# Optimization experiments

Hardware: AMD Instinct MI355X
Metric: run time of the kernel (lower is better)

Reference implementation:

```python
import jax, jax.numpy as jnp
import numpy as np

H = 2048        # hidden_size
NH = 16         # num query heads
NKV = 4         # num kv heads
HD = 128        # head_dim
EPS = 1e-6
SCALE = HD ** -0.5
GROUPS = NH // NKV


def rotate_half(x):
    x1, x2 = x[..., : HD // 2], x[..., HD // 2:]
    return jnp.concatenate((-x2, x1), axis=-1)


def rmsnorm(x, w):
    # x: [..., HD]
    var = jnp.mean(jnp.square(x), axis=-1, keepdims=True)
    return x * jax.lax.rsqrt(var + EPS) * w


def setup_inputs() -> dict:
    key = jax.random.key(0)
    ks = jax.random.split(key, 10)
    B, QL, CL = 4, 1024, 3072
    s = 0.02
    return {
        "noise": jax.random.normal(ks[0], (B, QL, H), jnp.float32),
        "ctx": jax.random.normal(ks[1], (B, CL, H), jnp.float32),
        "cos": jax.random.uniform(ks[2], (B, CL + QL, HD), jnp.float32, -1.0, 1.0),
        "sin": jax.random.uniform(ks[3], (B, CL + QL, HD), jnp.float32, -1.0, 1.0),
        "Wq": jax.random.normal(ks[4], (H, NH * HD), jnp.float32) * s,
        "Wk": jax.random.normal(ks[5], (H, NKV * HD), jnp.float32) * s,
        "Wv": jax.random.normal(ks[6], (H, NKV * HD), jnp.float32) * s,
        "Wo": jax.random.normal(ks[7], (NH * HD, H), jnp.float32) * s,
        "qn_w": jnp.ones((HD,), jnp.float32),
        "kn_w": jnp.ones((HD,), jnp.float32),
    }


def reference(noise, ctx, cos, sin, Wq, Wk, Wv, Wo, qn_w, kn_w):
    B, QL, _ = noise.shape
    CL = ctx.shape[1]
    KL = CL + QL

    # Q from noise
    q = (noise @ Wq).reshape(B, QL, NH, HD)
    q = rmsnorm(q, qn_w).transpose(0, 2, 1, 3)            # [B, NH, QL, HD]

    # K/V from [ctx ; noise]
    kv_in = jnp.concatenate([ctx, noise], axis=1)          # [B, KL, H]
    k = (kv_in @ Wk).reshape(B, KL, NKV, HD)
    k = rmsnorm(k, kn_w).transpose(0, 2, 1, 3)             # [B, NKV, KL, HD]
    v = (kv_in @ Wv).reshape(B, KL, NKV, HD).transpose(0, 2, 1, 3)

    # RoPE: queries use last QL positions
    cos_q, sin_q = cos[:, -QL:, None].transpose(0, 2, 1, 3), sin[:, -QL:, None].transpose(0, 2, 1, 3)
    cos_k, sin_k = cos[:, None], sin[:, None]
    q = q * cos_q + rotate_half(q) * sin_q
    k = k * cos_k + rotate_half(k) * sin_k

    # GQA expansion
    k = jnp.repeat(k, GROUPS, axis=1)                      # [B, NH, KL, HD]
    v = jnp.repeat(v, GROUPS, axis=1)

    attn = jnp.einsum('bhqd,bhkd->bhqk', q, k) * SCALE     # [B, NH, QL, KL]
    attn = jax.nn.softmax(attn.astype(jnp.float32), axis=-1).astype(v.dtype)
    out = jnp.einsum('bhqk,bhkd->bhqd', attn, v)
    out = out.transpose(0, 2, 1, 3).reshape(B, QL, NH * HD)
    return out @ Wo
```

## Files before the change

### kernel.cpp

```cpp
#include <hip/hip_runtime.h>
#include <cstdint>
#include <cstddef>

#define DEVI __device__ __forceinline__

typedef short bf16x8 __attribute__((ext_vector_type(8)));
typedef short bf16x4 __attribute__((ext_vector_type(4)));
typedef float f32x4  __attribute__((ext_vector_type(4)));

constexpr int H_  = 2048;
constexpr int NH  = 16;
constexpr int NKV = 4;
constexpr int HD  = 128;
constexpr int B_  = 4;
constexpr int QL  = 1024;
constexpr int CL  = 3072;
constexpr int KL  = 4096;
constexpr float EPS = 1e-6f;
constexpr float SCALE_LOG2E = 0.08838834764831845f * 1.4426950408889634f;

DEVI unsigned short f2bf(float x) {
  unsigned int u = __float_as_uint(x);
  u += 0x7FFFu + ((u >> 16) & 1u);
  return (unsigned short)(u >> 16);
}
DEVI float bf2f(unsigned short u) {
  return __uint_as_float(((unsigned int)u) << 16);
}
DEVI bf16x4 mk4(float a, float b, float c, float d) {
  unsigned ua = __float_as_uint(a) + 0x8000u, ub = __float_as_uint(b) + 0x8000u;
  unsigned uc = __float_as_uint(c) + 0x8000u, ud = __float_as_uint(d) + 0x8000u;
  union { unsigned u[2]; bf16x4 v; } r;
  r.u[0] = __builtin_amdgcn_perm(ub, ua, 0x07060302u);
  r.u[1] = __builtin_amdgcn_perm(ud, uc, 0x07060302u);
  return r.v;
}

DEVI void async16(const void* g, void* l) {
  __builtin_amdgcn_global_load_lds(
      (const __attribute__((address_space(1))) void*)g,
      (__attribute__((address_space(3))) void*)l, 16, 0, 0);
}

__global__ __launch_bounds__(256)
void prep(const float* __restrict__ noise, const float* __restrict__ ctx,
          unsigned short* __restrict__ kvin) {
  const size_t t = (size_t)blockIdx.x * 256 + threadIdx.x;
  const size_t e = t * 8;
  const int row = (int)(e / H_), col = (int)(e % H_);
  const int b = row >> 12, pos = row & 4095;
  const float* src = (pos < CL) ? ctx + ((size_t)(b * CL + pos)) * H_ + col
                                : noise + ((size_t)(b * QL + (pos - CL))) * H_ + col;
  float4 x = ((const float4*)src)[0], y = ((const float4*)src)[1];
  bf16x8 v;
  v[0] = (short)f2bf(x.x); v[1] = (short)f2bf(x.y);
  v[2] = (short)f2bf(x.z); v[3] = (short)f2bf(x.w);
  v[4] = (short)f2bf(y.x); v[5] = (short)f2bf(y.y);
  v[6] = (short)f2bf(y.z); v[7] = (short)f2bf(y.w);
  *(bf16x8*)(kvin + e) = v;
}

__global__ __launch_bounds__(256)
void wtrans(const float* __restrict__ in, unsigned short* __restrict__ out,
            int K, int N) {
  __shared__ float t[64][65];
  const int ktiles = K >> 6;
  const int kt = blockIdx.x % ktiles;
  const int nt = blockIdx.x / ktiles;
  {
    const int r = threadIdx.x >> 2, cs = threadIdx.x & 3;
    const float4* src = (const float4*)(in + (size_t)(kt * 64 + r) * N + nt * 64 + cs * 16);
    #pragma unroll
    for (int i = 0; i < 4; ++i) {
      float4 v = src[i];
      t[r][cs * 16 + i * 4 + 0] = v.x;
      t[r][cs * 16 + i * 4 + 1] = v.y;
      t[r][cs * 16 + i * 4 + 2] = v.z;
      t[r][cs * 16 + i * 4 + 3] = v.w;
    }
  }
  __syncthreads();
  {
    const int n = threadIdx.x >> 2, ks = threadIdx.x & 3;
    bf16x8 o0, o1;
    #pragma unroll
    for (int i = 0; i < 8; ++i) o0[i] = (short)f2bf(t[ks * 16 + i][n]);
    #pragma unroll
    for (int i = 0; i < 8; ++i) o1[i] = (short)f2bf(t[ks * 16 + 8 + i][n]);
    unsigned short* op = out + (size_t)(nt * 64 + n) * K + kt * 64 + ks * 16;
    *(bf16x8*)(op) = o0;
    *(bf16x8*)(op + 8) = o1;
  }
}

template <int MODE>
__global__ __launch_bounds__(256)
void gemm2(const unsigned short* __restrict__ Abf,
           const unsigned short* __restrict__ Bt,
           const float* __restrict__ normw,
           const float* __restrict__ cosb, const float* __restrict__ sinb,
           unsigned short* __restrict__ outb, float* __restrict__ outf) {
  constexpr int M  = (MODE == 1 || MODE == 2) ? (B_ * KL) : (B_ * QL);
  constexpr int K  = H_;
  constexpr int MT = M / 128;

  __shared__ union U {
    struct { unsigned short a[128][64]; unsigned short b[128][64]; } st;
    unsigned short ct[128][138];
  } sm;

  const int tid  = threadIdx.x;
  const int tm   = blockIdx.x % MT;
  const int tn   = blockIdx.x / MT;
  const int wid  = tid >> 6, lane = tid & 63, quad = lane >> 4, lm = lane & 15;
  const int wm   = wid >> 1, wn = wid & 1;

  f32x4 acc[4][4];
  #pragma unroll
  for (int i = 0; i < 4; ++i)
    #pragma unroll
    for (int j = 0; j < 4; ++j)
      #pragma unroll
      for (int r = 0; r < 4; ++r) acc[i][j][r] = 0.f;

  const unsigned short* agp[4];
  const unsigned short* bgp[4];
  #pragma unroll
  for (int i = 0; i < 4; ++i) {
    const int idx = i * 256 + tid;
    const int arow = idx >> 3, g = idx & 7, gg = g ^ (arow & 7);
    int grow;
    if constexpr (MODE == 0) {
      const int gmr = tm * 128 + arow;
      grow = (gmr >> 10) * KL + CL + (gmr & 1023);
    } else {
      grow = tm * 128 + arow;
    }
    agp[i] = Abf + (size_t)grow * K + gg * 8;
    bgp[i] = Bt + (size_t)(tn * 128 + arow) * K + gg * 8;
  }

  for (int kt = 0; kt < K / 64; ++kt) {
    __syncthreads();
    #pragma unroll
    for (int i = 0; i < 4; ++i) {
      async16(agp[i] + kt * 64, (char*)&sm.st.a[0][0] + (i * 256 + wid * 64) * 16);
      async16(bgp[i] + kt * 64, (char*)&sm.st.b[0][0] + (i * 256 + wid * 64) * 16);
    }
    __syncthreads();
    #pragma unroll
    for (int ks = 0; ks < 2; ++ks) {
      bf16x8 af[4], bfr[4];
      #pragma unroll
      for (int i = 0; i < 4; ++i) {
        const int swz = (ks * 4 + quad) ^ (lm & 7);
        af[i] = *(const bf16x8*)&sm.st.a[wm * 64 + i * 16 + lm][swz * 8];
      }
      #pragma unroll
      for (int j = 0; j < 4; ++j) {
        const int swz = (ks * 4 + quad) ^ (lm & 7);
        bfr[j] = *(const bf16x8*)&sm.st.b[wn * 64 + j * 16 + lm][swz * 8];
      }
      #pragma unroll
      for (int i = 0; i < 4; ++i)
        #pragma unroll
        for (int j = 0; j < 4; ++j)
          acc[i][j] = __builtin_amdgcn_mfma_f32_16x16x32_bf16(af[i], bfr[j], acc[i][j], 0, 0, 0);
    }
  }

  if constexpr (MODE == 3) {
    #pragma unroll
    for (int i = 0; i < 4; ++i)
      #pragma unroll
      for (int j = 0; j < 4; ++j) {
        const int row = tm * 128 + wm * 64 + i * 16 + quad * 4;
        const int col = tn * 128 + wn * 64 + j * 16 + lm;
        #pragma unroll
        for (int rr = 0; rr < 4; ++rr)
          outf[(size_t)(row + rr) * H_ + col] = acc[i][j][rr];
      }
    return;
  }

  __syncthreads();
  #pragma unroll
  for (int i = 0; i < 4; ++i)
    #pragma unroll
    for (int j = 0; j < 4; ++j)
      #pragma unroll
      for (int rr = 0; rr < 4; ++rr)
        sm.ct[wm * 64 + i * 16 + quad * 4 + rr][wn * 64 + j * 16 + lm] =
            f2bf(acc[i][j][rr]);
  __syncthreads();

  const int row2 = tid >> 1, half = tid & 1;
  if constexpr (MODE == 0 || MODE == 1) {
    const int gmr = tm * 128 + row2;
    int ci; size_t obase;
    if constexpr (MODE == 0) {
      const int b = gmr >> 10, pos = gmr & 1023;
      ci = (b * KL + CL + pos) * HD;
      obase = ((size_t)((b * NH + tn) * QL + pos)) * HD;
    } else {
      const int b = gmr >> 12, pos = gmr & 4095;
      ci = (b * KL + pos) * HD;
      obase = ((size_t)((b * NKV + tn) * KL + pos)) * HD;
    }
    float ss = 0.f;
    for (int d = half * 64; d < half * 64 + 64; ++d) {
      float v = bf2f(sm.ct[row2][d]);
      ss += v * v;
    }
    ss += __shfl_xor(ss, 1);
    const float rinv = rsqrtf(ss * (1.0f / 128.0f) + EPS);
    constexpr float OSC = (MODE == 0) ? SCALE_LOG2E : 1.0f;
    #pragma unroll
    for (int d8 = 0; d8 < 8; ++d8) {
      bf16x8 v;
      #pragma unroll
      for (int j = 0; j < 8; ++j) {
        const int d = half * 64 + d8 * 8 + j;
        const float x  = bf2f(sm.ct[row2][d])      * rinv * normw[d];
        const float xo = bf2f(sm.ct[row2][d ^ 64]) * rinv * normw[d ^ 64];
        const float rot = (d < 64) ? -xo : xo;
        v[j] = (short)f2bf((x * cosb[ci + d] + rot * sinb[ci + d]) * OSC);
      }
      *(bf16x8*)(outb + obase + half * 64 + d8 * 8) = v;
    }
  } else {
    const int d = row2;
    const int b = (tm * 128) >> 12;
    const int posBase = ((tm * 128) & 4095) + half * 64;
    const size_t obase = ((size_t)((b * NKV + tn) * HD + d)) * KL + posBase;
    #pragma unroll
    for (int k8 = 0; k8 < 8; ++k8) {
      bf16x8 v;
      #pragma unroll
      for (int j = 0; j < 8; ++j)
        v[j] = (short)sm.ct[half * 64 + k8 * 8 + j][d];
      *(bf16x8*)(outb + obase + k8 * 8) = v;
    }
  }
}

__global__ __launch_bounds__(256, 1)
void attn2(const unsigned short* __restrict__ qb,
           const unsigned short* __restrict__ kb,
           const unsigned short* __restrict__ vtb,
           unsigned short* __restrict__ ao) {
  __shared__ unsigned short kl[2][64][128];
  __shared__ unsigned short vl[2][128][64];

  const int tid = threadIdx.x;
  const int wave = tid >> 6, lane = tid & 63, quad = lane >> 4, lm = lane & 15;
  const int qblk = blockIdx.x & 3;
  const int bh = blockIdx.x >> 2;
  const int b = bh >> 4, h = bh & 15, kvh = h >> 2;
  const int q0 = qblk * 256 + wave * 64;

  bf16x8 qf[4][4];
  const unsigned short* qbase = qb + ((size_t)((b * NH + h) * QL + q0)) * HD;
  #pragma unroll
  for (int t = 0; t < 4; ++t)
    #pragma unroll
    for (int kq = 0; kq < 4; ++kq)
      qf[t][kq] = *(const bf16x8*)(qbase + (t * 16 + lm) * HD + kq * 32 + quad * 8);

  f32x4 o[4][8];
  float li[4] = {0.f, 0.f, 0.f, 0.f};
  #pragma unroll
  for (int t = 0; t < 4; ++t)
    #pragma unroll
    for (int dt = 0; dt < 8; ++dt)
      #pragma unroll
      for (int rr = 0; rr < 4; ++rr) o[t][dt][rr] = 0.f;

  const unsigned short* kbase = kb + ((size_t)(b * NKV + kvh)) * KL * HD;
  const unsigned short* vbase = vtb + ((size_t)(b * NKV + kvh)) * HD * KL;

  const int krow0 = tid >> 4, kgc = tid & 15;
  const int kgg = (kgc & 8) | ((kgc & 7) ^ (krow0 & 7));
  const unsigned short* kgp0 = kbase + (size_t)krow0 * HD + kgg * 8;
  const int vrow0 = tid >> 3;
  const int vgv = (tid & 7) ^ (vrow0 & 7);
  const unsigned short* vgp0 = vbase + (size_t)vrow0 * KL + vgv * 8;

  auto stage = [&](int bufi, int ktt) {
    #pragma unroll
    for (int i = 0; i < 4; ++i) {
      async16(kgp0 + (size_t)ktt * (64 * HD) + i * (16 * HD),
              (char*)&kl[bufi][0][0] + (i * 256 + wave * 64) * 16);
      async16(vgp0 + (size_t)ktt * 64 + i * (32 * KL),
              (char*)&vl[bufi][0][0] + (i * 256 + wave * 64) * 16);
    }
  };

  stage(0, 0);
  for (int kt = 0; kt < KL / 64; ++kt) {
    const int cur = kt & 1;
    if (kt + 1 < KL / 64) {
      stage(cur ^ 1, kt + 1);
      asm volatile("s_waitcnt vmcnt(8)" ::: "memory");
    } else {
      asm volatile("s_waitcnt vmcnt(0)" ::: "memory");
    }
    __builtin_amdgcn_s_barrier();

    #pragma unroll
    for (int nt = 0; nt < 4; ++nt) {
      bf16x8 kf[4];
      #pragma unroll
      for (int kq = 0; kq < 4; ++kq) {
        const int gc = kq * 4 + quad;
        const int swz = (gc & 8) | ((gc & 7) ^ (lm & 7));
        kf[kq] = *(const bf16x8*)&kl[cur][nt * 16 + lm][swz * 8];
      }
      bf16x4 vf[8];
      #pragma unroll
      for (int dt = 0; dt < 8; ++dt) {
        const int gv = (nt * 2 + (quad >> 1)) ^ (lm & 7);
        vf[dt] = *(const bf16x4*)&vl[cur][dt * 16 + lm][gv * 8 + (quad & 1) * 4];
      }
      f32x4 s[4];
      #pragma unroll
      for (int t = 0; t < 4; ++t)
        #pragma unroll
        for (int rr = 0; rr < 4; ++rr) s[t][rr] = 0.f;
      #pragma unroll
      for (int kq = 0; kq < 4; ++kq)
        #pragma unroll
        for (int t = 0; t < 4; ++t)
          s[t] = __builtin_amdgcn_mfma_f32_16x16x32_bf16(kf[kq], qf[t][kq], s[t], 0, 0, 0);
      #pragma unroll
      for (int t = 0; t < 4; ++t) {
        float e0 = __builtin_amdgcn_exp2f(s[t][0]);
        float e1 = __builtin_amdgcn_exp2f(s[t][1]);
        float e2 = __builtin_amdgcn_exp2f(s[t][2]);
        float e3 = __builtin_amdgcn_exp2f(s[t][3]);
        li[t] += (e0 + e1) + (e2 + e3);
        bf16x4 p = mk4(e0, e1, e2, e3);
        #pragma unroll
        for (int dt = 0; dt < 8; ++dt)
          o[t][dt] = __builtin_amdgcn_mfma_f32_16x16x16bf16_1k(vf[dt], p, o[t][dt], 0, 0, 0);
      }
    }
    __builtin_amdgcn_s_barrier();
  }

  #pragma unroll
  for (int t = 0; t < 4; ++t) {
    float l = li[t];
    l += __shfl_xor(l, 16);
    l += __shfl_xor(l, 32);
    const float inv = 1.0f / l;
    const size_t rowbase = ((size_t)(b * QL + q0 + t * 16 + lm)) * (NH * HD) + h * HD;
    #pragma unroll
    for (int dt = 0; dt < 8; ++dt) {
      bf16x4 v = mk4(o[t][dt][0] * inv, o[t][dt][1] * inv,
                     o[t][dt][2] * inv, o[t][dt][3] * inv);
      *(bf16x4*)(ao + rowbase + dt * 16 + quad * 4) = v;
    }
  }
}

extern "C" void kernel_launch(void* const* d_in, const int* in_sizes, int n_in,
                              void* d_out, int out_size, void* d_ws, size_t ws_size,
                              hipStream_t stream) {
  const float* noise = (const float*)d_in[0];
  const float* ctx   = (const float*)d_in[1];
  const float* cosb  = (const float*)d_in[2];
  const float* sinb  = (const float*)d_in[3];
  const float* Wq    = (const float*)d_in[4];
  const float* Wk    = (const float*)d_in[5];
  const float* Wv    = (const float*)d_in[6];
  const float* Wo    = (const float*)d_in[7];
  const float* qn    = (const float*)d_in[8];
  const float* kn    = (const float*)d_in[9];
  float* out = (float*)d_out;

  char* ws = (char*)d_ws;
  unsigned short* kvin = (unsigned short*)(ws);
  unsigned short* aob  = (unsigned short*)(ws);
  unsigned short* WqT  = (unsigned short*)(ws + 67108864);
  unsigned short* WkT  = (unsigned short*)(ws + 67108864 + 8388608);
  unsigned short* WvT  = (unsigned short*)(ws + 67108864 + 10485760);
  unsigned short* WoT  = (unsigned short*)(ws + 67108864 + 12582912);
  unsigned short* qbuf = (unsigned short*)(ws + 67108864 + 20971520);
  unsigned short* kbuf = (unsigned short*)(ws + 67108864 + 37748736);
  unsigned short* vtb  = (unsigned short*)(ws + 67108864 + 54525952);

  prep<<<dim3((B_ * KL * H_) / 8 / 256), dim3(256), 0, stream>>>(noise, ctx, kvin);

  wtrans<<<dim3(1024), dim3(256), 0, stream>>>(Wq, WqT, 2048, 2048);
  wtrans<<<dim3(256),  dim3(256), 0, stream>>>(Wk, WkT, 2048, 512);
  wtrans<<<dim3(256),  dim3(256), 0, stream>>>(Wv, WvT, 2048, 512);
  wtrans<<<dim3(1024), dim3(256), 0, stream>>>(Wo, WoT, 2048, 2048);

  gemm2<0><<<dim3(32 * 16), dim3(256), 0, stream>>>(
      kvin, WqT, qn, cosb, sinb, qbuf, nullptr);
  gemm2<1><<<dim3(128 * 4), dim3(256), 0, stream>>>(
      kvin, WkT, kn, cosb, sinb, kbuf, nullptr);
  gemm2<2><<<dim3(128 * 4), dim3(256), 0, stream>>>(
      kvin, WvT, nullptr, nullptr, nullptr, vtb, nullptr);

  attn2<<<dim3(256), dim3(256), 0, stream>>>(qbuf, kbuf, vtb, aob);

  gemm2<3><<<dim3(32 * 16), dim3(256), 0, stream>>>(
      aob, WoT, nullptr, nullptr, nullptr, nullptr, out);
}
```

Before: 636.3 us.

## Halve attention query tile, double occupancy, use K=32 MFMA for PV

```diff
diff --git a/kernel.cpp b/kernel.cpp
--- a/kernel.cpp
+++ b/kernel.cpp
@@ -27,12 +27,14 @@
 DEVI float bf2f(unsigned short u) {
   return __uint_as_float(((unsigned int)u) << 16);
 }
+DEVI unsigned mk2(float a, float b) {
+  unsigned ua = __float_as_uint(a) + 0x8000u, ub = __float_as_uint(b) + 0x8000u;
+  return __builtin_amdgcn_perm(ub, ua, 0x07060302u);
+}
 DEVI bf16x4 mk4(float a, float b, float c, float d) {
-  unsigned ua = __float_as_uint(a) + 0x8000u, ub = __float_as_uint(b) + 0x8000u;
-  unsigned uc = __float_as_uint(c) + 0x8000u, ud = __float_as_uint(d) + 0x8000u;
   union { unsigned u[2]; bf16x4 v; } r;
-  r.u[0] = __builtin_amdgcn_perm(ub, ua, 0x07060302u);
-  r.u[1] = __builtin_amdgcn_perm(ud, uc, 0x07060302u);
+  r.u[0] = mk2(a, b);
+  r.u[1] = mk2(c, d);
   return r.v;
 }
 
@@ -244,7 +246,7 @@
   }
 }
 
-__global__ __launch_bounds__(256, 1)
+__global__ __launch_bounds__(256, 2)
 void attn2(const unsigned short* __restrict__ qb,
            const unsigned short* __restrict__ kb,
            const unsigned short* __restrict__ vtb,
@@ -254,23 +256,24 @@
 
   const int tid = threadIdx.x;
   const int wave = tid >> 6, lane = tid & 63, quad = lane >> 4, lm = lane & 15;
-  const int qblk = blockIdx.x & 3;
-  const int bh = blockIdx.x >> 2;
+  const int qblk = blockIdx.x & 7;
+  const int bh = blockIdx.x >> 3;
   const int b = bh >> 4, h = bh & 15, kvh = h >> 2;
-  const int q0 = qblk * 256 + wave * 64;
-
-  bf16x8 qf[4][4];
+  const int q0 = qblk * 128 + wave * 32;
+  const bool qodd = (quad & 1) != 0;
+
+  bf16x8 qf[2][4];
   const unsigned short* qbase = qb + ((size_t)((b * NH + h) * QL + q0)) * HD;
   #pragma unroll
-  for (int t = 0; t < 4; ++t)
+  for (int t = 0; t < 2; ++t)
     #pragma unroll
     for (int kq = 0; kq < 4; ++kq)
       qf[t][kq] = *(const bf16x8*)(qbase + (t * 16 + lm) * HD + kq * 32 + quad * 8);
 
-  f32x4 o[4][8];
-  float li[4] = {0.f, 0.f, 0.f, 0.f};
-  #pragma unroll
-  for (int t = 0; t < 4; ++t)
+  f32x4 o[2][8];
+  float li[2] = {0.f, 0.f};
+  #pragma unroll
+  for (int t = 0; t < 2; ++t)
     #pragma unroll
     for (int dt = 0; dt < 8; ++dt)
       #pragma unroll
@@ -308,48 +311,68 @@
     __builtin_amdgcn_s_barrier();
 
     #pragma unroll
-    for (int nt = 0; nt < 4; ++nt) {
-      bf16x8 kf[4];
-      #pragma unroll
-      for (int kq = 0; kq < 4; ++kq) {
-        const int gc = kq * 4 + quad;
-        const int swz = (gc & 8) | ((gc & 7) ^ (lm & 7));
-        kf[kq] = *(const bf16x8*)&kl[cur][nt * 16 + lm][swz * 8];
-      }
-      bf16x4 vf[8];
+    for (int j = 0; j < 2; ++j) {
+      unsigned pk[2][2][2];
+      #pragma unroll
+      for (int sub = 0; sub < 2; ++sub) {
+        const int nt = j * 2 + sub;
+        bf16x8 kf[4];
+        #pragma unroll
+        for (int kq = 0; kq < 4; ++kq) {
+          const int gc = kq * 4 + quad;
+          const int swz = (gc & 8) | ((gc & 7) ^ (lm & 7));
+          kf[kq] = *(const bf16x8*)&kl[cur][nt * 16 + lm][swz * 8];
+        }
+        f32x4 s0 = {0.f, 0.f, 0.f, 0.f}, s1 = {0.f, 0.f, 0.f, 0.f};
+        __builtin_amdgcn_s_setprio(1);
+        #pragma unroll
+        for (int kq = 0; kq < 4; ++kq) {
+          s0 = __builtin_amdgcn_mfma_f32_16x16x32_bf16(kf[kq], qf[0][kq], s0, 0, 0, 0);
+          s1 = __builtin_amdgcn_mfma_f32_16x16x32_bf16(kf[kq], qf[1][kq], s1, 0, 0, 0);
+        }
+        __builtin_amdgcn_s_setprio(0);
+        float e00 = __builtin_amdgcn_exp2f(s0[0]), e01 = __builtin_amdgcn_exp2f(s0[1]);
+        float e02 = __builtin_amdgcn_exp2f(s0[2]), e03 = __builtin_amdgcn_exp2f(s0[3]);
+        float e10 = __builtin_amdgcn_exp2f(s1[0]), e11 = __builtin_amdgcn_exp2f(s1[1]);
+        float e12 = __builtin_amdgcn_exp2f(s1[2]), e13 = __builtin_amdgcn_exp2f(s1[3]);
+        li[0] += (e00 + e01) + (e02 + e03);
+        li[1] += (e10 + e11) + (e12 + e13);
+        pk[0][sub][0] = mk2(e00, e01); pk[0][sub][1] = mk2(e02, e03);
+        pk[1][sub][0] = mk2(e10, e11); pk[1][sub][1] = mk2(e12, e13);
+      }
+      bf16x8 P[2];
+      #pragma unroll
+      for (int t = 0; t < 2; ++t) {
+        unsigned a0 = pk[t][0][0], b0 = pk[t][1][0];
+        unsigned a1 = pk[t][0][1], b1 = pk[t][1][1];
+        asm volatile("v_permlane32_swap_b32 %0, %1" : "+v"(a0), "+v"(b0));
+        asm volatile("v_permlane32_swap_b32 %0, %1" : "+v"(a1), "+v"(b1));
+        const unsigned sa0 = __builtin_amdgcn_ds_swizzle(a0, 0x401F);
+        const unsigned sb0 = __builtin_amdgcn_ds_swizzle(b0, 0x401F);
+        const unsigned sa1 = __builtin_amdgcn_ds_swizzle(a1, 0x401F);
+        const unsigned sb1 = __builtin_amdgcn_ds_swizzle(b1, 0x401F);
+        union { unsigned u[4]; bf16x8 v; } up;
+        up.u[0] = qodd ? sb0 : a0;
+        up.u[1] = qodd ? sb1 : a1;
+        up.u[2] = qodd ? b0 : sa0;
+        up.u[3] = qodd ? b1 : sa1;
+        P[t] = up.v;
+      }
+      __builtin_amdgcn_s_setprio(1);
       #pragma unroll
       for (int dt = 0; dt < 8; ++dt) {
-        const int gv = (nt * 2 + (quad >> 1)) ^ (lm & 7);
-        vf[dt] = *(const bf16x4*)&vl[cur][dt * 16 + lm][gv * 8 + (quad & 1) * 4];
-      }
-      f32x4 s[4];
-      #pragma unroll
-      for (int t = 0; t < 4; ++t)
-        #pragma unroll
-        for (int rr = 0; rr < 4; ++rr) s[t][rr] = 0.f;
-      #pragma unroll
-      for (int kq = 0; kq < 4; ++kq)
-        #pragma unroll
-        for (int t = 0; t < 4; ++t)
-          s[t] = __builtin_amdgcn_mfma_f32_16x16x32_bf16(kf[kq], qf[t][kq], s[t], 0, 0, 0);
-      #pragma unroll
-      for (int t = 0; t < 4; ++t) {
-        float e0 = __builtin_amdgcn_exp2f(s[t][0]);
-        float e1 = __builtin_amdgcn_exp2f(s[t][1]);
-        float e2 = __builtin_amdgcn_exp2f(s[t][2]);
-        float e3 = __builtin_amdgcn_exp2f(s[t][3]);
-        li[t] += (e0 + e1) + (e2 + e3);
-        bf16x4 p = mk4(e0, e1, e2, e3);
-        #pragma unroll
-        for (int dt = 0; dt < 8; ++dt)
-          o[t][dt] = __builtin_amdgcn_mfma_f32_16x16x16bf16_1k(vf[dt], p, o[t][dt], 0, 0, 0);
-      }
+        const int gv = (j * 4 + quad) ^ (lm & 7);
+        bf16x8 vfr = *(const bf16x8*)&vl[cur][dt * 16 + lm][gv * 8];
+        o[0][dt] = __builtin_amdgcn_mfma_f32_16x16x32_bf16(vfr, P[0], o[0][dt], 0, 0, 0);
+        o[1][dt] = __builtin_amdgcn_mfma_f32_16x16x32_bf16(vfr, P[1], o[1][dt], 0, 0, 0);
+      }
+      __builtin_amdgcn_s_setprio(0);
     }
     __builtin_amdgcn_s_barrier();
   }
 
   #pragma unroll
-  for (int t = 0; t < 4; ++t) {
+  for (int t = 0; t < 2; ++t) {
     float l = li[t];
     l += __shfl_xor(l, 16);
     l += __shfl_xor(l, 32);
@@ -404,7 +427,7 @@
   gemm2<2><<<dim3(128 * 4), dim3(256), 0, stream>>>(
       kvin, WvT, nullptr, nullptr, nullptr, vtb, nullptr);
 
-  attn2<<<dim3(256), dim3(256), 0, stream>>>(qbuf, kbuf, vtb, aob);
+  attn2<<<dim3(512), dim3(256), 0, stream>>>(qbuf, kbuf, vtb, aob);
 
   gemm2<3><<<dim3(32 * 16), dim3(256), 0, stream>>>(
       aob, WoT, nullptr, nullptr, nullptr, nullptr, out);
```

New measurement: 584.3 us. 1.09x faster.

## Use 16x16x32 MFMA for PV via permlane-swapped P fragments

Applied to the files above, without the earlier changes.

```diff
diff --git a/kernel.cpp b/kernel.cpp
--- a/kernel.cpp
+++ b/kernel.cpp
@@ -27,12 +27,15 @@
 DEVI float bf2f(unsigned short u) {
   return __uint_as_float(((unsigned int)u) << 16);
 }
+DEVI unsigned cvtpk(float a, float b) {
+  unsigned r;
+  asm("v_cvt_pk_bf16_f32 %0, %1, %2" : "=v"(r) : "v"(a), "v"(b));
+  return r;
+}
 DEVI bf16x4 mk4(float a, float b, float c, float d) {
-  unsigned ua = __float_as_uint(a) + 0x8000u, ub = __float_as_uint(b) + 0x8000u;
-  unsigned uc = __float_as_uint(c) + 0x8000u, ud = __float_as_uint(d) + 0x8000u;
   union { unsigned u[2]; bf16x4 v; } r;
-  r.u[0] = __builtin_amdgcn_perm(ub, ua, 0x07060302u);
-  r.u[1] = __builtin_amdgcn_perm(ud, uc, 0x07060302u);
+  r.u[0] = cvtpk(a, b);
+  r.u[1] = cvtpk(c, d);
   return r.v;
 }
 
@@ -308,42 +311,74 @@
     __builtin_amdgcn_s_barrier();
 
     #pragma unroll
-    for (int nt = 0; nt < 4; ++nt) {
-      bf16x8 kf[4];
-      #pragma unroll
-      for (int kq = 0; kq < 4; ++kq) {
-        const int gc = kq * 4 + quad;
-        const int swz = (gc & 8) | ((gc & 7) ^ (lm & 7));
-        kf[kq] = *(const bf16x8*)&kl[cur][nt * 16 + lm][swz * 8];
-      }
-      bf16x4 vf[8];
+    for (int j = 0; j < 2; ++j) {
+      bf16x8 kf[2][4];
+      #pragma unroll
+      for (int sub = 0; sub < 2; ++sub) {
+        const int nt = j * 2 + sub;
+        #pragma unroll
+        for (int kq = 0; kq < 4; ++kq) {
+          const int gc = kq * 4 + quad;
+          const int swz = (gc & 8) | ((gc & 7) ^ (lm & 7));
+          kf[sub][kq] = *(const bf16x8*)&kl[cur][nt * 16 + lm][swz * 8];
+        }
+      }
+      f32x4 s[4][2];
+      #pragma unroll
+      for (int t = 0; t < 4; ++t)
+        #pragma unroll
+        for (int sub = 0; sub < 2; ++sub)
+          #pragma unroll
+          for (int rr = 0; rr < 4; ++rr) s[t][sub][rr] = 0.f;
+      __builtin_amdgcn_s_setprio(1);
+      #pragma unroll
+      for (int kq = 0; kq < 4; ++kq)
+        #pragma unroll
+        for (int sub = 0; sub < 2; ++sub)
+          #pragma unroll
+          for (int t = 0; t < 4; ++t)
+            s[t][sub] = __builtin_amdgcn_mfma_f32_16x16x32_bf16(
+                kf[sub][kq], qf[t][kq], s[t][sub], 0, 0, 0);
+      __builtin_amdgcn_s_setprio(0);
+
+      bf16x8 vfr[8];
       #pragma unroll
       for (int dt = 0; dt < 8; ++dt) {
-        const int gv = (nt * 2 + (quad >> 1)) ^ (lm & 7);
-        vf[dt] = *(const bf16x4*)&vl[cur][dt * 16 + lm][gv * 8 + (quad & 1) * 4];
-      }
-      f32x4 s[4];
-      #pragma unroll
-      for (int t = 0; t < 4; ++t)
-        #pragma unroll
-        for (int rr = 0; rr < 4; ++rr) s[t][rr] = 0.f;
-      #pragma unroll
-      for (int kq = 0; kq < 4; ++kq)
+        const int gv = (j * 4 + quad) ^ (lm & 7);
+        vfr[dt] = *(const bf16x8*)&vl[cur][dt * 16 + lm][gv * 8];
+      }
+
+      bf16x8 P[4];
+      #pragma unroll
+      for (int t = 0; t < 4; ++t) {
+        float e00 = __builtin_amdgcn_exp2f(s[t][0][0]);
+        float e01 = __builtin_amdgcn_exp2f(s[t][0][1]);
+        float e02 = __builtin_amdgcn_exp2f(s[t][0][2]);
+        float e03 = __builtin_amdgcn_exp2f(s[t][0][3]);
+        float e10 = __builtin_amdgcn_exp2f(s[t][1][0]);
+        float e11 = __builtin_amdgcn_exp2f(s[t][1][1]);
+        float e12 = __builtin_amdgcn_exp2f(s[t][1][2]);
+        float e13 = __builtin_amdgcn_exp2f(s[t][1][3]);
+        li[t] += ((e00 + e01) + (e02 + e03)) + ((e10 + e11) + (e12 + e13));
+        unsigned A0 = cvtpk(e00, e01), A1 = cvtpk(e02, e03);
+        unsigned B0 = cvtpk(e10, e11), B1 = cvtpk(e12, e13);
+        asm volatile("v_permlane32_swap_b32 %0, %1" : "+v"(A0), "+v"(B0));
+        asm volatile("v_permlane32_swap_b32 %0, %1" : "+v"(A1), "+v"(B1));
+        asm volatile("v_permlane16_swap_b32 %0, %1" : "+v"(A0), "+v"(B0));
+        asm volatile("v_permlane16_swap_b32 %0, %1" : "+v"(A1), "+v"(B1));
+        union { unsigned u[4]; bf16x8 v; } up;
+        up.u[0] = A0; up.u[1] = A1; up.u[2] = B0; up.u[3] = B1;
+        P[t] = up.v;
+      }
+
+      __builtin_amdgcn_s_setprio(1);
+      #pragma unroll
+      for (int dt = 0; dt < 8; ++dt)
         #pragma unroll
         for (int t = 0; t < 4; ++t)
-          s[t] = __builtin_amdgcn_mfma_f32_16x16x32_bf16(kf[kq], qf[t][kq], s[t], 0, 0, 0);
-      #pragma unroll
-      for (int t = 0; t < 4; ++t) {
-        float e0 = __builtin_amdgcn_exp2f(s[t][0]);
-        float e1 = __builtin_amdgcn_exp2f(s[t][1]);
-        float e2 = __builtin_amdgcn_exp2f(s[t][2]);
-        float e3 = __builtin_amdgcn_exp2f(s[t][3]);
-        li[t] += (e0 + e1) + (e2 + e3);
-        bf16x4 p = mk4(e0, e1, e2, e3);
-        #pragma unroll
-        for (int dt = 0; dt < 8; ++dt)
-          o[t][dt] = __builtin_amdgcn_mfma_f32_16x16x16bf16_1k(vf[dt], p, o[t][dt], 0, 0, 0);
-      }
+          o[t][dt] = __builtin_amdgcn_mfma_f32_16x16x32_bf16(
+              vfr[dt], P[t], o[t][dt], 0, 0, 0);
+      __builtin_amdgcn_s_setprio(0);
     }
     __builtin_amdgcn_s_barrier();
   }
```

After: 614.5 us. 1.04x faster.
